# Optimization experiments

Measured on AMD Instinct MI355X. Metric: run time of the kernel, lower is better.

## Reference

```python
import jax, jax.numpy as jnp
import numpy as np

N_HEAD = 12
HEAD_DIM = 64
N_EMBD = 768
ATTN_MULT = 0.125
B, T = 2, 2048
NEG_INF = -1e30


def setup_inputs() -> dict:
    key = jax.random.key(0)
    ks = jax.random.split(key, 3)
    x = jax.random.normal(ks[0], (B, T, N_EMBD), dtype=jnp.float32)
    W_attn = jax.random.normal(ks[1], (N_EMBD, 3 * N_HEAD * HEAD_DIM), dtype=jnp.float32) * 0.02
    b_attn = jnp.zeros((3 * N_HEAD * HEAD_DIM,), dtype=jnp.float32)
    W_proj = jax.random.normal(ks[2], (N_HEAD * HEAD_DIM, N_EMBD), dtype=jnp.float32) * 0.02
    b_proj = jnp.zeros((N_EMBD,), dtype=jnp.float32)
    return {"x": x, "W_attn": W_attn, "b_attn": b_attn, "W_proj": W_proj, "b_proj": b_proj}


def reference(x, W_attn, b_attn, W_proj, b_proj):
    Bsz, Tlen, C = x.shape
    H, D = N_HEAD, HEAD_DIM
    qkv = x @ W_attn + b_attn                       # [B,T,3*H*D]
    q, k, v = jnp.split(qkv, 3, axis=-1)
    q = q.reshape(Bsz, Tlen, H, D).transpose(0, 2, 1, 3)   # [B,H,T,D]
    k = k.reshape(Bsz, Tlen, H, D).transpose(0, 2, 1, 3)
    v = v.reshape(Bsz, Tlen, H, D).transpose(0, 2, 1, 3)

    att = jnp.einsum('bhtd,bhsd->bhts', q, k) * ATTN_MULT  # [B,H,T,T]
    causal = jnp.tril(jnp.ones((Tlen, Tlen), dtype=bool))  # [T,T]
    att = jnp.where(causal, att, NEG_INF)

    # selection mask from head 0 (SelectionHeadLinearComboKind.NONE)
    S = jax.nn.relu(att[:, 0:1, :, :])                     # [B,1,T,T]; relu kills -inf
    # protect_bos_token: zero column 0 (key index 0)
    col = jnp.arange(Tlen)
    S = S * (col[None, None, None, :] != 0)
    # prevent_from_masking_myself: zero diagonal
    S = S * (1.0 - jnp.eye(Tlen, dtype=S.dtype))

    # accumulate selection over query (row) axis: ProtectionKind.NONE
    FF = jnp.cumsum(S, axis=-2)                            # [B,1,T,T]
    att = att - FF                                         # broadcast over heads

    p = jax.nn.softmax(att, axis=-1)                       # [B,H,T,T]
    y = jnp.einsum('bhts,bhsd->bhtd', p, v)                # [B,H,T,D]
    y = y.transpose(0, 2, 1, 3).reshape(Bsz, Tlen, H * D)  # [B,T,H*D]
    return y @ W_proj + b_proj
```

## Files before the change

kernel.cpp:

```cpp
#include <hip/hip_runtime.h>
#include <math.h>

#define T 2048
#define NH 12
#define HD 64
#define C3 2304
#define CE 768
#define NB 2

typedef __attribute__((ext_vector_type(8))) short bf16x8;
typedef __attribute__((ext_vector_type(4))) float f32x4;
typedef __attribute__((ext_vector_type(16))) float f32x16;
typedef __attribute__((ext_vector_type(4))) unsigned u32x4;

__device__ __forceinline__ void gload16(const void* g, void* l) {
    __builtin_amdgcn_global_load_lds(
        (const __attribute__((address_space(1))) void*)g,
        (__attribute__((address_space(3))) void*)l, 16, 0, 0);
}

__device__ inline void bf16split(float a, unsigned short& h, unsigned short& l) {
    unsigned int u = __float_as_uint(a);
    unsigned int r = (u + 0x7FFFu + ((u >> 16) & 1u)) >> 16;
    h = (unsigned short)r;
    float hf = __uint_as_float(r << 16);
    float lo = a - hf;
    unsigned int v = __float_as_uint(lo);
    l = (unsigned short)((v + 0x7FFFu + ((v >> 16) & 1u)) >> 16);
}

__device__ inline void packP(float a, float b, unsigned& wh, unsigned& wl) {
    unsigned short ha, la, hb, lb;
    bf16split(a, ha, la); bf16split(b, hb, lb);
    wh = (unsigned)ha | ((unsigned)hb << 16);
    wl = (unsigned)la | ((unsigned)lb << 16);
}

__global__ __launch_bounds__(256) void cvt_split_kernel(const float* __restrict__ A,
        unsigned short* __restrict__ H, unsigned short* __restrict__ L) {
    int i = blockIdx.x * 256 + threadIdx.x;
    float4 a0 = *(reinterpret_cast<const float4*>(A) + (size_t)i * 2);
    float4 a1 = *(reinterpret_cast<const float4*>(A) + (size_t)i * 2 + 1);
    float f[8] = {a0.x, a0.y, a0.z, a0.w, a1.x, a1.y, a1.z, a1.w};
    unsigned short h[8], l[8];
    #pragma unroll
    for (int j = 0; j < 8; ++j) bf16split(f[j], h[j], l[j]);
    uint4 hv, lv;
    hv.x = (unsigned)h[0] | ((unsigned)h[1] << 16); hv.y = (unsigned)h[2] | ((unsigned)h[3] << 16);
    hv.z = (unsigned)h[4] | ((unsigned)h[5] << 16); hv.w = (unsigned)h[6] | ((unsigned)h[7] << 16);
    lv.x = (unsigned)l[0] | ((unsigned)l[1] << 16); lv.y = (unsigned)l[2] | ((unsigned)l[3] << 16);
    lv.z = (unsigned)l[4] | ((unsigned)l[5] << 16); lv.w = (unsigned)l[6] | ((unsigned)l[7] << 16);
    reinterpret_cast<uint4*>(H)[i] = hv;
    reinterpret_cast<uint4*>(L)[i] = lv;
}

__global__ __launch_bounds__(256) void cvt_split_T_kernel(const float* __restrict__ W,
        unsigned short* __restrict__ H, unsigned short* __restrict__ L, int K, int N) {
    __shared__ float tile[64][65];
    const int n0 = blockIdx.x * 64, k0 = blockIdx.y * 64;
    const int t = threadIdx.x;
    {
        int r = t >> 2, c4 = (t & 3) * 16;
        #pragma unroll
        for (int u = 0; u < 4; ++u) {
            float4 w = *reinterpret_cast<const float4*>(&W[(size_t)(k0 + r) * N + n0 + c4 + u * 4]);
            tile[r][c4 + u * 4 + 0] = w.x; tile[r][c4 + u * 4 + 1] = w.y;
            tile[r][c4 + u * 4 + 2] = w.z; tile[r][c4 + u * 4 + 3] = w.w;
        }
    }
    __syncthreads();
    {
        int n = t >> 2, kc = (t & 3) * 16;
        unsigned short h[16], l[16];
        #pragma unroll
        for (int j = 0; j < 16; ++j) bf16split(tile[kc + j][n], h[j], l[j]);
        uint4 hv0, hv1, lv0, lv1;
        hv0.x = (unsigned)h[0] | ((unsigned)h[1] << 16);  hv0.y = (unsigned)h[2] | ((unsigned)h[3] << 16);
        hv0.z = (unsigned)h[4] | ((unsigned)h[5] << 16);  hv0.w = (unsigned)h[6] | ((unsigned)h[7] << 16);
        hv1.x = (unsigned)h[8] | ((unsigned)h[9] << 16);  hv1.y = (unsigned)h[10] | ((unsigned)h[11] << 16);
        hv1.z = (unsigned)h[12] | ((unsigned)h[13] << 16); hv1.w = (unsigned)h[14] | ((unsigned)h[15] << 16);
        lv0.x = (unsigned)l[0] | ((unsigned)l[1] << 16);  lv0.y = (unsigned)l[2] | ((unsigned)l[3] << 16);
        lv0.z = (unsigned)l[4] | ((unsigned)l[5] << 16);  lv0.w = (unsigned)l[6] | ((unsigned)l[7] << 16);
        lv1.x = (unsigned)l[8] | ((unsigned)l[9] << 16);  lv1.y = (unsigned)l[10] | ((unsigned)l[11] << 16);
        lv1.z = (unsigned)l[12] | ((unsigned)l[13] << 16); lv1.w = (unsigned)l[14] | ((unsigned)l[15] << 16);
        size_t o = (size_t)(n0 + n) * K + k0 + kc;
        reinterpret_cast<uint4*>(&H[o])[0] = hv0; reinterpret_cast<uint4*>(&H[o])[1] = hv1;
        reinterpret_cast<uint4*>(&L[o])[0] = lv0; reinterpret_cast<uint4*>(&L[o])[1] = lv1;
    }
}

__global__ __launch_bounds__(256) void cvt_kv_vt_kernel(const float* __restrict__ Vtmp,
        unsigned short* __restrict__ Vh, unsigned short* __restrict__ Vl) {
    __shared__ float tile[64][65];
    const int s0 = blockIdx.x * 64;
    const int bh = blockIdx.y;
    const int tid = threadIdx.x;
    {
        int r = tid >> 2, c0 = (tid & 3) * 16;
        const float* src = Vtmp + ((size_t)bh * T + s0 + r) * 64 + c0;
        #pragma unroll
        for (int u = 0; u < 4; ++u) {
            float4 w = *reinterpret_cast<const float4*>(src + u * 4);
            tile[r][c0 + u * 4 + 0] = w.x; tile[r][c0 + u * 4 + 1] = w.y;
            tile[r][c0 + u * 4 + 2] = w.z; tile[r][c0 + u * 4 + 3] = w.w;
        }
    }
    __syncthreads();
    {
        int d = tid >> 2, cs = (tid & 3) * 16;
        unsigned short hh[16], ll[16];
        #pragma unroll
        for (int j = 0; j < 16; ++j) bf16split(tile[cs + j][d], hh[j], ll[j]);
        uint4 hv0, hv1, lv0, lv1;
        hv0.x = (unsigned)hh[0] | ((unsigned)hh[1] << 16);  hv0.y = (unsigned)hh[2] | ((unsigned)hh[3] << 16);
        hv0.z = (unsigned)hh[4] | ((unsigned)hh[5] << 16);  hv0.w = (unsigned)hh[6] | ((unsigned)hh[7] << 16);
        hv1.x = (unsigned)hh[8] | ((unsigned)hh[9] << 16);  hv1.y = (unsigned)hh[10] | ((unsigned)hh[11] << 16);
        hv1.z = (unsigned)hh[12] | ((unsigned)hh[13] << 16); hv1.w = (unsigned)hh[14] | ((unsigned)hh[15] << 16);
        lv0.x = (unsigned)ll[0] | ((unsigned)ll[1] << 16);  lv0.y = (unsigned)ll[2] | ((unsigned)ll[3] << 16);
        lv0.z = (unsigned)ll[4] | ((unsigned)ll[5] << 16);  lv0.w = (unsigned)ll[6] | ((unsigned)ll[7] << 16);
        lv1.x = (unsigned)ll[8] | ((unsigned)ll[9] << 16);  lv1.y = (unsigned)ll[10] | ((unsigned)ll[11] << 16);
        lv1.z = (unsigned)ll[12] | ((unsigned)ll[13] << 16); lv1.w = (unsigned)ll[14] | ((unsigned)ll[15] << 16);
        size_t o = ((size_t)bh * 64 + d) * T + s0 + cs;
        reinterpret_cast<uint4*>(&Vh[o])[0] = hv0; reinterpret_cast<uint4*>(&Vh[o])[1] = hv1;
        reinterpret_cast<uint4*>(&Vl[o])[0] = lv0; reinterpret_cast<uint4*>(&Vl[o])[1] = lv1;
    }
}

#define LD32 32
__global__ __launch_bounds__(256) void gemm_mfma_kernel(
        const unsigned short* __restrict__ Ah, const unsigned short* __restrict__ Al,
        const unsigned short* __restrict__ Bh, const unsigned short* __restrict__ Bl,
        const float* __restrict__ bias, float* __restrict__ Cm,
        int M, int N, int K) {
    __shared__ unsigned short lA[2][128 * LD32];
    __shared__ unsigned short lB[2][128 * LD32];
    const int tid = threadIdx.x;
    const int nwg = gridDim.x * gridDim.y;
    int bid = blockIdx.y * gridDim.x + blockIdx.x;
    bid = (bid & 7) * (nwg >> 3) + (bid >> 3);
    const int bm = (bid / gridDim.x) * 128, bn = (bid % gridDim.x) * 128;
    const int lane = tid & 63, wid = tid >> 6;
    const int wr = wid >> 1, wc = wid & 1;
    f32x4 acc[4][4];
    #pragma unroll
    for (int i = 0; i < 4; ++i)
        #pragma unroll
        for (int j = 0; j < 4; ++j) acc[i][j] = (f32x4){0.f, 0.f, 0.f, 0.f};
    const int srow0 = wid * 32 + (lane >> 2);
    const int scn   = lane & 3;
    const int arb = wr * 64 + (lane & 15);
    const int brb = wc * 64 + (lane & 15);
    const int kc  = lane >> 4;
    for (int k0 = 0; k0 < K; k0 += 32) {
        __syncthreads();
        #pragma unroll
        for (int h = 0; h < 2; ++h) {
            int row = srow0 + h * 16;
            int cs = scn ^ ((row >> 1) & 3);
            size_t ao = (size_t)(bm + row) * K + k0 + cs * 8;
            size_t bo = (size_t)(bn + row) * K + k0 + cs * 8;
            unsigned short* d0 = &lA[0][(wid * 32 + h * 16) * LD32];
            unsigned short* d1 = &lA[1][(wid * 32 + h * 16) * LD32];
            unsigned short* d2 = &lB[0][(wid * 32 + h * 16) * LD32];
            unsigned short* d3 = &lB[1][(wid * 32 + h * 16) * LD32];
            gload16(&Ah[ao], d0);
            gload16(&Al[ao], d1);
            gload16(&Bh[bo], d2);
            gload16(&Bl[bo], d3);
        }
        __syncthreads();
        bf16x8 fa[2][4], fb[2][4];
        #pragma unroll
        for (int fi = 0; fi < 4; ++fi) {
            int ra = arb + fi * 16, rb = brb + fi * 16;
            int ca = (kc ^ ((ra >> 1) & 3)) * 8;
            int cb = (kc ^ ((rb >> 1) & 3)) * 8;
            fa[0][fi] = *reinterpret_cast<const bf16x8*>(&lA[0][ra * LD32 + ca]);
            fa[1][fi] = *reinterpret_cast<const bf16x8*>(&lA[1][ra * LD32 + ca]);
            fb[0][fi] = *reinterpret_cast<const bf16x8*>(&lB[0][rb * LD32 + cb]);
            fb[1][fi] = *reinterpret_cast<const bf16x8*>(&lB[1][rb * LD32 + cb]);
        }
        #pragma unroll
        for (int fi = 0; fi < 4; ++fi)
            #pragma unroll
            for (int fj = 0; fj < 4; ++fj) {
                acc[fi][fj] = __builtin_amdgcn_mfma_f32_16x16x32_bf16(fb[0][fj], fa[0][fi], acc[fi][fj], 0, 0, 0);
                acc[fi][fj] = __builtin_amdgcn_mfma_f32_16x16x32_bf16(fb[0][fj], fa[1][fi], acc[fi][fj], 0, 0, 0);
                acc[fi][fj] = __builtin_amdgcn_mfma_f32_16x16x32_bf16(fb[1][fj], fa[0][fi], acc[fi][fj], 0, 0, 0);
            }
    }
    const int mloc = lane & 15, ng = (lane >> 4) * 4;
    #pragma unroll
    for (int fi = 0; fi < 4; ++fi) {
        int row = bm + wr * 64 + fi * 16 + mloc;
        #pragma unroll
        for (int fj = 0; fj < 4; ++fj) {
            int n0 = bn + wc * 64 + fj * 16 + ng;
            float4 bv = *reinterpret_cast<const float4*>(&bias[n0]);
            float4 o4 = {acc[fi][fj][0] + bv.x, acc[fi][fj][1] + bv.y,
                         acc[fi][fj][2] + bv.z, acc[fi][fj][3] + bv.w};
            *reinterpret_cast<float4*>(&Cm[(size_t)row * N + n0]) = o4;
        }
    }
}

__global__ __launch_bounds__(256) void gemm_qkv_mfma_kernel(
        const unsigned short* __restrict__ Ah, const unsigned short* __restrict__ Al,
        const unsigned short* __restrict__ Bh, const unsigned short* __restrict__ Bl,
        const float* __restrict__ bias,
        unsigned short* __restrict__ Qh, unsigned short* __restrict__ Ql,
        unsigned short* __restrict__ Kh, unsigned short* __restrict__ Kl,
        float* __restrict__ Vtmp) {
    const int K = CE;
    __shared__ unsigned short lA[2][128 * LD32];
    __shared__ unsigned short lB[2][128 * LD32];
    const int tid = threadIdx.x;
    const int nwg = gridDim.x * gridDim.y;
    int bid = blockIdx.y * gridDim.x + blockIdx.x;
    bid = (bid & 7) * (nwg >> 3) + (bid >> 3);
    const int bm = (bid / gridDim.x) * 128, bn = (bid % gridDim.x) * 128;
    const int lane = tid & 63, wid = tid >> 6;
    const int wr = wid >> 1, wc = wid & 1;
    f32x4 acc[4][4];
    #pragma unroll
    for (int i = 0; i < 4; ++i)
        #pragma unroll
        for (int j = 0; j < 4; ++j) acc[i][j] = (f32x4){0.f, 0.f, 0.f, 0.f};
    const int srow0 = wid * 32 + (lane >> 2);
    const int scn   = lane & 3;
    const int arb = wr * 64 + (lane & 15);
    const int brb = wc * 64 + (lane & 15);
    const int kc  = lane >> 4;
    for (int k0 = 0; k0 < K; k0 += 32) {
        __syncthreads();
        #pragma unroll
        for (int h = 0; h < 2; ++h) {
            int row = srow0 + h * 16;
            int cs = scn ^ ((row >> 1) & 3);
            size_t ao = (size_t)(bm + row) * K + k0 + cs * 8;
            size_t bo = (size_t)(bn + row) * K + k0 + cs * 8;
            unsigned short* d0 = &lA[0][(wid * 32 + h * 16) * LD32];
            unsigned short* d1 = &lA[1][(wid * 32 + h * 16) * LD32];
            unsigned short* d2 = &lB[0][(wid * 32 + h * 16) * LD32];
            unsigned short* d3 = &lB[1][(wid * 32 + h * 16) * LD32];
            gload16(&Ah[ao], d0);
            gload16(&Al[ao], d1);
            gload16(&Bh[bo], d2);
            gload16(&Bl[bo], d3);
        }
        __syncthreads();
        bf16x8 fa[2][4], fb[2][4];
        #pragma unroll
        for (int fi = 0; fi < 4; ++fi) {
            int ra = arb + fi * 16, rb = brb + fi * 16;
            int ca = (kc ^ ((ra >> 1) & 3)) * 8;
            int cb = (kc ^ ((rb >> 1) & 3)) * 8;
            fa[0][fi] = *reinterpret_cast<const bf16x8*>(&lA[0][ra * LD32 + ca]);
            fa[1][fi] = *reinterpret_cast<const bf16x8*>(&lA[1][ra * LD32 + ca]);
            fb[0][fi] = *reinterpret_cast<const bf16x8*>(&lB[0][rb * LD32 + cb]);
            fb[1][fi] = *reinterpret_cast<const bf16x8*>(&lB[1][rb * LD32 + cb]);
        }
        #pragma unroll
        for (int fi = 0; fi < 4; ++fi)
            #pragma unroll
            for (int fj = 0; fj < 4; ++fj) {
                acc[fi][fj] = __builtin_amdgcn_mfma_f32_16x16x32_bf16(fb[0][fj], fa[0][fi], acc[fi][fj], 0, 0, 0);
                acc[fi][fj] = __builtin_amdgcn_mfma_f32_16x16x32_bf16(fb[0][fj], fa[1][fi], acc[fi][fj], 0, 0, 0);
                acc[fi][fj] = __builtin_amdgcn_mfma_f32_16x16x32_bf16(fb[1][fj], fa[0][fi], acc[fi][fj], 0, 0, 0);
            }
    }
    const int colbase = bn + wc * 64;
    const int region = colbase / 768;
    const int h = (colbase % 768) >> 6;
    const int mloc = lane & 15, ng = (lane >> 4) * 4;
    #pragma unroll
    for (int fi = 0; fi < 4; ++fi) {
        int tg = bm + wr * 64 + fi * 16 + mloc;
        int bb = tg >> 11, t = tg & (T - 1);
        #pragma unroll
        for (int fj = 0; fj < 4; ++fj) {
            int dbase = fj * 16 + ng;
            float4 bv = *reinterpret_cast<const float4*>(&bias[colbase + dbase]);
            float v0 = acc[fi][fj][0] + bv.x, v1 = acc[fi][fj][1] + bv.y;
            float v2 = acc[fi][fj][2] + bv.z, v3 = acc[fi][fj][3] + bv.w;
            size_t o = ((size_t)(bb * NH + h) * T + t) * 64 + dbase;
            if (region == 2) {
                float4 o4 = {v0, v1, v2, v3};
                *reinterpret_cast<float4*>(&Vtmp[o]) = o4;
            } else {
                unsigned short hh[4], ll[4];
                bf16split(v0, hh[0], ll[0]); bf16split(v1, hh[1], ll[1]);
                bf16split(v2, hh[2], ll[2]); bf16split(v3, hh[3], ll[3]);
                uint2 ph = {(unsigned)hh[0] | ((unsigned)hh[1] << 16),
                            (unsigned)hh[2] | ((unsigned)hh[3] << 16)};
                uint2 pl = {(unsigned)ll[0] | ((unsigned)ll[1] << 16),
                            (unsigned)ll[2] | ((unsigned)ll[3] << 16)};
                if (region == 0) {
                    *reinterpret_cast<uint2*>(&Qh[o]) = ph;
                    *reinterpret_cast<uint2*>(&Ql[o]) = pl;
                } else {
                    *reinterpret_cast<uint2*>(&Kh[o]) = ph;
                    *reinterpret_cast<uint2*>(&Kl[o]) = pl;
                }
            }
        }
    }
}

__global__ __launch_bounds__(256) void gemm_bias_kernel(
        const float* __restrict__ A, const float* __restrict__ B,
        const float* __restrict__ bias, float* __restrict__ Cm,
        int M, int N, int K) {
    __shared__ float As[16][64];
    __shared__ float Bs[16][68];
    const int tid = threadIdx.x;
    const int ty = tid >> 4, tx = tid & 15;
    const int bm = blockIdx.y * 64, bn = blockIdx.x * 64;
    float acc[4][4] = {};
    for (int k0 = 0; k0 < K; k0 += 16) {
        {
            int r = tid >> 2;
            int kk = (tid & 3) * 4;
            float4 a = *reinterpret_cast<const float4*>(&A[(size_t)(bm + r) * K + k0 + kk]);
            As[kk + 0][r] = a.x; As[kk + 1][r] = a.y; As[kk + 2][r] = a.z; As[kk + 3][r] = a.w;
        }
        {
            int kk = tid >> 4;
            int c = (tid & 15) * 4;
            *reinterpret_cast<float4*>(&Bs[kk][c]) =
                *reinterpret_cast<const float4*>(&B[(size_t)(k0 + kk) * N + bn + c]);
        }
        __syncthreads();
        #pragma unroll
        for (int kk = 0; kk < 16; ++kk) {
            float4 a4 = *reinterpret_cast<const float4*>(&As[kk][ty * 4]);
            float4 b4 = *reinterpret_cast<const float4*>(&Bs[kk][tx * 4]);
            float av[4] = {a4.x, a4.y, a4.z, a4.w};
            float bv[4] = {b4.x, b4.y, b4.z, b4.w};
            #pragma unroll
            for (int i = 0; i < 4; ++i)
                #pragma unroll
                for (int j = 0; j < 4; ++j)
                    acc[i][j] = fmaf(av[i], bv[j], acc[i][j]);
        }
        __syncthreads();
    }
    #pragma unroll
    for (int i = 0; i < 4; ++i) {
        int row = bm + ty * 4 + i;
        #pragma unroll
        for (int j = 0; j < 4; ++j) {
            int col = bn + tx * 4 + j;
            Cm[(size_t)row * N + col] = acc[i][j] + bias[col];
        }
    }
}

#define FST 72

__global__ __launch_bounds__(256) void s0_mfma_kernel(
        const unsigned short* __restrict__ Qh, const unsigned short* __restrict__ Ql,
        const unsigned short* __restrict__ Kh, const unsigned short* __restrict__ Kl,
        float* __restrict__ S, float* __restrict__ Psum) {
    const int kb = blockIdx.x * 64, qb = blockIdx.y * 64, b = blockIdx.z;
    const int tid = threadIdx.x;
    float* Sb = S + (size_t)b * T * T;
    if (kb > qb) {
        const int ty = tid >> 4, tx = tid & 15;
        #pragma unroll
        for (int i = 0; i < 4; ++i) {
            float4 z = {0.f, 0.f, 0.f, 0.f};
            *reinterpret_cast<float4*>(&Sb[(size_t)(qb + ty * 4 + i) * T + kb + tx * 4]) = z;
        }
        if (tid < 64) Psum[((size_t)(b * 32 + (qb >> 6)) * T) + kb + tid] = 0.f;
        return;
    }
    const int lane = tid & 63, w = tid >> 6;
    const int fr = lane & 15, fg = lane >> 4;
    __shared__ unsigned short Ks[2][64 * FST];
    __shared__ float csum[4][64];
    const int hb0 = b * NH;
    {
        const int sr = tid >> 2, sc0 = (tid & 3) * 16;
        const unsigned short* kh = Kh + ((size_t)hb0 * T + kb + sr) * 64 + sc0;
        const unsigned short* kl = Kl + ((size_t)hb0 * T + kb + sr) * 64 + sc0;
        uint4 a0 = reinterpret_cast<const uint4*>(kh)[0];
        uint4 a1 = reinterpret_cast<const uint4*>(kh)[1];
        uint4 b0 = reinterpret_cast<const uint4*>(kl)[0];
        uint4 b1 = reinterpret_cast<const uint4*>(kl)[1];
        *reinterpret_cast<uint4*>(&Ks[0][sr * FST + sc0 + 0]) = a0;
        *reinterpret_cast<uint4*>(&Ks[0][sr * FST + sc0 + 8]) = a1;
        *reinterpret_cast<uint4*>(&Ks[1][sr * FST + sc0 + 0]) = b0;
        *reinterpret_cast<uint4*>(&Ks[1][sr * FST + sc0 + 8]) = b1;
    }
    bf16x8 qh[2], ql[2];
    #pragma unroll
    for (int ks = 0; ks < 2; ++ks) {
        size_t qo = ((size_t)hb0 * T + qb + w * 16 + fr) * 64 + ks * 32 + fg * 8;
        qh[ks] = *reinterpret_cast<const bf16x8*>(&Qh[qo]);
        ql[ks] = *reinterpret_cast<const bf16x8*>(&Ql[qo]);
    }
    __syncthreads();
    f32x4 qk[4];
    #pragma unroll
    for (int fj = 0; fj < 4; ++fj) qk[fj] = (f32x4){0.f, 0.f, 0.f, 0.f};
    #pragma unroll
    for (int ks = 0; ks < 2; ++ks) {
        bf16x8 kbh[4], kbl[4];
        #pragma unroll
        for (int fj = 0; fj < 4; ++fj) {
            kbh[fj] = *reinterpret_cast<const bf16x8*>(&Ks[0][(fj * 16 + fr) * FST + ks * 32 + fg * 8]);
            kbl[fj] = *reinterpret_cast<const bf16x8*>(&Ks[1][(fj * 16 + fr) * FST + ks * 32 + fg * 8]);
        }
        #pragma unroll
        for (int fj = 0; fj < 4; ++fj) {
            qk[fj] = __builtin_amdgcn_mfma_f32_16x16x32_bf16(qh[ks], kbh[fj], qk[fj], 0, 0, 0);
            qk[fj] = __builtin_amdgcn_mfma_f32_16x16x32_bf16(qh[ks], kbl[fj], qk[fj], 0, 0, 0);
            qk[fj] = __builtin_amdgcn_mfma_f32_16x16x32_bf16(ql[ks], kbh[fj], qk[fj], 0, 0, 0);
        }
    }
    float colsum[4] = {0.f, 0.f, 0.f, 0.f};
    #pragma unroll
    for (int p = 0; p < 4; ++p) {
        int t = qb + w * 16 + fg * 4 + p;
        #pragma unroll
        for (int fj = 0; fj < 4; ++fj) {
            int s = kb + fj * 16 + fr;
            float v = qk[fj][p] * 0.125f;
            float o = (s >= 1 && s < t) ? fmaxf(v, 0.0f) : 0.0f;
            Sb[(size_t)t * T + s] = o;
            colsum[fj] += o;
        }
    }
    #pragma unroll
    for (int fj = 0; fj < 4; ++fj) {
        colsum[fj] += __shfl_xor(colsum[fj], 16);
        colsum[fj] += __shfl_xor(colsum[fj], 32);
    }
    if (lane < 16) {
        #pragma unroll
        for (int fj = 0; fj < 4; ++fj) csum[w][fj * 16 + lane] = colsum[fj];
    }
    __syncthreads();
    if (tid < 64) {
        float v = csum[0][tid] + csum[1][tid] + csum[2][tid] + csum[3][tid];
        Psum[((size_t)(b * 32 + (qb >> 6)) * T) + kb + tid] = v;
    }
}

__global__ __launch_bounds__(256) void s0_kernel(const float* __restrict__ qkv,
                                                 float* __restrict__ S) {
    const int kb = blockIdx.x * 64, qb = blockIdx.y * 64, b = blockIdx.z;
    const int tid = threadIdx.x, ty = tid >> 4, tx = tid & 15;
    float* Sb = S + (size_t)b * T * T;
    if (kb > qb) {
        #pragma unroll
        for (int i = 0; i < 4; ++i) {
            int row = qb + ty * 4 + i;
            float4 z = {0.f, 0.f, 0.f, 0.f};
            *reinterpret_cast<float4*>(&Sb[(size_t)row * T + kb + tx * 4]) = z;
        }
        return;
    }
    __shared__ float Qt[64][68];
    __shared__ float Kt[64][68];
    {
        int r = tid >> 2;
        int c0 = (tid & 3) * 16;
        const float* qrow = qkv + (size_t)(b * T + qb + r) * C3 + 0;
        const float* krow = qkv + (size_t)(b * T + kb + r) * C3 + 768;
        #pragma unroll
        for (int u = 0; u < 4; ++u) {
            float4 q4 = *reinterpret_cast<const float4*>(&qrow[c0 + u * 4]);
            float4 k4 = *reinterpret_cast<const float4*>(&krow[c0 + u * 4]);
            int d = c0 + u * 4;
            Qt[d + 0][r] = q4.x; Qt[d + 1][r] = q4.y; Qt[d + 2][r] = q4.z; Qt[d + 3][r] = q4.w;
            Kt[d + 0][r] = k4.x; Kt[d + 1][r] = k4.y; Kt[d + 2][r] = k4.z; Kt[d + 3][r] = k4.w;
        }
    }
    __syncthreads();
    float acc[4][4] = {};
    #pragma unroll
    for (int d = 0; d < 64; ++d) {
        float4 qv = *reinterpret_cast<const float4*>(&Qt[d][ty * 4]);
        float4 kv = *reinterpret_cast<const float4*>(&Kt[d][tx * 4]);
        float qa[4] = {qv.x, qv.y, qv.z, qv.w};
        float ka[4] = {kv.x, kv.y, kv.z, kv.w};
        #pragma unroll
        for (int i = 0; i < 4; ++i)
            #pragma unroll
            for (int j = 0; j < 4; ++j)
                acc[i][j] = fmaf(qa[i], ka[j], acc[i][j]);
    }
    #pragma unroll
    for (int i = 0; i < 4; ++i) {
        int t = qb + ty * 4 + i;
        float o[4];
        #pragma unroll
        for (int j = 0; j < 4; ++j) {
            int s = kb + tx * 4 + j;
            float v = acc[i][j] * 0.125f;
            o[j] = (s >= 1 && s < t) ? fmaxf(v, 0.0f) : 0.0f;
        }
        float4 o4 = {o[0], o[1], o[2], o[3]};
        *reinterpret_cast<float4*>(&Sb[(size_t)t * T + kb + tx * 4]) = o4;
    }
}

__global__ __launch_bounds__(256) void colsum_kernel(const float* __restrict__ S,
                                                     float* __restrict__ Psum) {
    int s = blockIdx.x * 256 + threadIdx.x;
    int j = blockIdx.y, b = blockIdx.z;
    const float* Sb = S + (size_t)b * T * T;
    float sum = 0.f;
    for (int r = 0; r < 64; ++r) sum += Sb[(size_t)(j * 64 + r) * T + s];
    Psum[((size_t)b * 32 + j) * T + s] = sum;
}

__global__ __launch_bounds__(256) void scanseg_kernel(float* __restrict__ Psum) {
    int s = blockIdx.x * 256 + threadIdx.x;
    int b = blockIdx.y;
    float v[32];
    #pragma unroll
    for (int j = 0; j < 32; ++j)
        v[j] = Psum[((size_t)(b * 32 + j)) * T + s];
    float run = 0.f;
    #pragma unroll
    for (int j = 0; j < 32; ++j) {
        Psum[((size_t)(b * 32 + j)) * T + s] = run;
        run += v[j];
    }
}

__global__ __launch_bounds__(256) void ffscan_kernel(float* __restrict__ S,
                                                     const float* __restrict__ Psum) {
    int s = blockIdx.x * 256 + threadIdx.x;
    int j = blockIdx.y, b = blockIdx.z;
    float run = Psum[((size_t)b * 32 + j) * T + s];
    float* Sb = S + (size_t)b * T * T;
    for (int r = 0; r < 64; ++r) {
        size_t idx = (size_t)(j * 64 + r) * T + s;
        run += Sb[idx];
        Sb[idx] = run;
    }
}

__device__ const int FTQ[40] = {15,15,15,15,14,14,14,13,13,13,12,12,12,11,11,11,10,10,9,9,8,8,7,7,6,5,4,3,14,10,6,2,13,9,5,1,12,8,4,0};
__device__ const int FK0[40] = {0,8,16,24,0,8,16,0,8,16,0,8,16,0,8,16,0,8,0,8,0,8,0,8,0,0,0,0,24,16,8,0,24,16,8,0,24,16,8,0};
__device__ const int FK1[40] = {8,16,24,32,8,16,24,8,16,24,8,16,24,8,16,24,8,16,8,16,8,16,8,16,8,8,8,8,30,22,14,6,28,20,12,4,26,18,10,2};
__device__ const int FCB[12] = {0,2,4,6,8,11,14,17,20,24,28,32};

__global__ __launch_bounds__(256) void flash_mfma_kernel(
        const unsigned short* __restrict__ Qh, const unsigned short* __restrict__ Ql,
        const unsigned short* __restrict__ Kh, const unsigned short* __restrict__ Kl,
        const unsigned short* __restrict__ Vth, const unsigned short* __restrict__ Vtl,
        const float* __restrict__ FF,
        unsigned short* __restrict__ Yh, unsigned short* __restrict__ Yl,
        float* __restrict__ PART) {
    const int hb = blockIdx.x;
    const int h = hb % NH, b = hb / NH;
    const int u = blockIdx.y;
    const int tq = FTQ[u], kt0 = FK0[u], kt1 = FK1[u];
    const int qb = tq * 128;
    const int tid = threadIdx.x;
    const int lane = tid & 63, w = tid >> 6;
    const int q31 = lane & 31, hi = lane >> 5;
    const int trow = qb + w * 32 + q31;
    __shared__ unsigned short KS[2][64 * FST];
    __shared__ unsigned short VS[2][64 * FST];

    bf16x8 qfh[4], qfl[4];
    #pragma unroll
    for (int dblk = 0; dblk < 4; ++dblk) {
        size_t qo = ((size_t)hb * T + trow) * 64 + dblk * 16 + hi * 8;
        qfh[dblk] = *reinterpret_cast<const bf16x8*>(&Qh[qo]);
        qfl[dblk] = *reinterpret_cast<const bf16x8*>(&Ql[qo]);
    }

    f32x16 oacc0 = (f32x16)(0.f), oacc1 = (f32x16)(0.f);
    float m = -1e30f, l = 0.f;
    const float* FFb = FF + (size_t)b * T * T;
    const int sr = tid >> 2, sc0 = (tid & 3) * 16;

    for (int kt = kt0; kt < kt1; ++kt) {
        const int kb = kt * 64;
        __syncthreads();
        {
            const unsigned short* ksrc = Kh + ((size_t)hb * T + kb + sr) * 64 + sc0;
            const unsigned short* ksrl = Kl + ((size_t)hb * T + kb + sr) * 64 + sc0;
            const unsigned short* vsrc = Vth + ((size_t)hb * 64 + sr) * T + kb + sc0;
            const unsigned short* vsrl = Vtl + ((size_t)hb * 64 + sr) * T + kb + sc0;
            uint4 k0v = reinterpret_cast<const uint4*>(ksrc)[0];
            uint4 k1v = reinterpret_cast<const uint4*>(ksrc)[1];
            uint4 k2v = reinterpret_cast<const uint4*>(ksrl)[0];
            uint4 k3v = reinterpret_cast<const uint4*>(ksrl)[1];
            uint4 v0v = reinterpret_cast<const uint4*>(vsrc)[0];
            uint4 v1v = reinterpret_cast<const uint4*>(vsrc)[1];
            uint4 v2v = reinterpret_cast<const uint4*>(vsrl)[0];
            uint4 v3v = reinterpret_cast<const uint4*>(vsrl)[1];
            *reinterpret_cast<uint4*>(&KS[0][sr * FST + sc0 + 0]) = k0v;
            *reinterpret_cast<uint4*>(&KS[0][sr * FST + sc0 + 8]) = k1v;
            *reinterpret_cast<uint4*>(&KS[1][sr * FST + sc0 + 0]) = k2v;
            *reinterpret_cast<uint4*>(&KS[1][sr * FST + sc0 + 8]) = k3v;
            *reinterpret_cast<uint4*>(&VS[0][sr * FST + sc0 + 0]) = v0v;
            *reinterpret_cast<uint4*>(&VS[0][sr * FST + sc0 + 8]) = v1v;
            *reinterpret_cast<uint4*>(&VS[1][sr * FST + sc0 + 0]) = v2v;
            *reinterpret_cast<uint4*>(&VS[1][sr * FST + sc0 + 8]) = v3v;
        }
        __syncthreads();
        f32x16 acc[2];
        acc[0] = (f32x16)(0.f); acc[1] = (f32x16)(0.f);
        #pragma unroll
        for (int sb = 0; sb < 2; ++sb) {
            #pragma unroll
            for (int dblk = 0; dblk < 4; ++dblk) {
                bf16x8 kfh = *reinterpret_cast<const bf16x8*>(&KS[0][(sb * 32 + q31) * FST + dblk * 16 + hi * 8]);
                bf16x8 kfl = *reinterpret_cast<const bf16x8*>(&KS[1][(sb * 32 + q31) * FST + dblk * 16 + hi * 8]);
                acc[sb] = __builtin_amdgcn_mfma_f32_32x32x16_bf16(kfh, qfh[dblk], acc[sb], 0, 0, 0);
                acc[sb] = __builtin_amdgcn_mfma_f32_32x32x16_bf16(kfh, qfl[dblk], acc[sb], 0, 0, 0);
                acc[sb] = __builtin_amdgcn_mfma_f32_32x32x16_bf16(kfl, qfh[dblk], acc[sb], 0, 0, 0);
            }
        }
        float pv[2][16];
        #pragma unroll
        for (int sb = 0; sb < 2; ++sb) {
            #pragma unroll
            for (int g = 0; g < 4; ++g) {
                float4 f4 = *reinterpret_cast<const float4*>(
                    &FFb[(size_t)trow * T + kb + sb * 32 + g * 8 + hi * 4]);
                float fv[4] = {f4.x, f4.y, f4.z, f4.w};
                #pragma unroll
                for (int a = 0; a < 4; ++a) {
                    int r = g * 4 + a;
                    int s = kb + sb * 32 + a + g * 8 + hi * 4;
                    float val = acc[sb][r] * 0.125f - fv[a];
                    pv[sb][r] = (s <= trow) ? val : -1e30f;
                }
            }
        }
        float tm = pv[0][0];
        #pragma unroll
        for (int sb = 0; sb < 2; ++sb)
            #pragma unroll
            for (int r = 0; r < 16; ++r) tm = fmaxf(tm, pv[sb][r]);
        tm = fmaxf(tm, __shfl_xor(tm, 32));
        float mn = fmaxf(m, tm);
        float scale = __expf(m - mn);
        float rs = 0.f;
        #pragma unroll
        for (int sb = 0; sb < 2; ++sb)
            #pragma unroll
            for (int r = 0; r < 16; ++r) {
                float pe = __expf(pv[sb][r] - mn);
                pv[sb][r] = pe; rs += pe;
            }
        rs += __shfl_xor(rs, 32);
        l = l * scale + rs;
        m = mn;
        oacc0 *= scale; oacc1 *= scale;
        unsigned wh[2][4][2], wl[2][4][2];
        #pragma unroll
        for (int sb = 0; sb < 2; ++sb)
            #pragma unroll
            for (int bq = 0; bq < 4; ++bq)
                #pragma unroll
                for (int h2 = 0; h2 < 2; ++h2)
                    packP(pv[sb][4 * bq + 2 * h2], pv[sb][4 * bq + 2 * h2 + 1],
                          wh[sb][bq][h2], wl[sb][bq][h2]);
        #pragma unroll
        for (int kk = 0; kk < 4; ++kk) {
            const int sb = kk >> 1;
            const int b0 = 2 * (kk & 1), b1 = b0 + 1;
            unsigned sh_b1_0 = (unsigned)__shfl_xor((int)wh[sb][b1][0], 32);
            unsigned sh_b1_1 = (unsigned)__shfl_xor((int)wh[sb][b1][1], 32);
            unsigned sh_b0_0 = (unsigned)__shfl_xor((int)wh[sb][b0][0], 32);
            unsigned sh_b0_1 = (unsigned)__shfl_xor((int)wh[sb][b0][1], 32);
            unsigned sl_b1_0 = (unsigned)__shfl_xor((int)wl[sb][b1][0], 32);
            unsigned sl_b1_1 = (unsigned)__shfl_xor((int)wl[sb][b1][1], 32);
            unsigned sl_b0_0 = (unsigned)__shfl_xor((int)wl[sb][b0][0], 32);
            unsigned sl_b0_1 = (unsigned)__shfl_xor((int)wl[sb][b0][1], 32);
            u32x4 th, tl;
            th[0] = hi ? sh_b1_0 : wh[sb][b0][0];
            th[1] = hi ? sh_b1_1 : wh[sb][b0][1];
            th[2] = hi ? wh[sb][b1][0] : sh_b0_0;
            th[3] = hi ? wh[sb][b1][1] : sh_b0_1;
            tl[0] = hi ? sl_b1_0 : wl[sb][b0][0];
            tl[1] = hi ? sl_b1_1 : wl[sb][b0][1];
            tl[2] = hi ? wl[sb][b1][0] : sl_b0_0;
            tl[3] = hi ? wl[sb][b1][1] : sl_b0_1;
            bf16x8 pbh = __builtin_bit_cast(bf16x8, th);
            bf16x8 pbl = __builtin_bit_cast(bf16x8, tl);
            {
                bf16x8 vfh = *reinterpret_cast<const bf16x8*>(&VS[0][(q31) * FST + kk * 16 + hi * 8]);
                bf16x8 vfl = *reinterpret_cast<const bf16x8*>(&VS[1][(q31) * FST + kk * 16 + hi * 8]);
                oacc0 = __builtin_amdgcn_mfma_f32_32x32x16_bf16(vfh, pbh, oacc0, 0, 0, 0);
                oacc0 = __builtin_amdgcn_mfma_f32_32x32x16_bf16(vfh, pbl, oacc0, 0, 0, 0);
                oacc0 = __builtin_amdgcn_mfma_f32_32x32x16_bf16(vfl, pbh, oacc0, 0, 0, 0);
            }
            {
                bf16x8 vfh = *reinterpret_cast<const bf16x8*>(&VS[0][(32 + q31) * FST + kk * 16 + hi * 8]);
                bf16x8 vfl = *reinterpret_cast<const bf16x8*>(&VS[1][(32 + q31) * FST + kk * 16 + hi * 8]);
                oacc1 = __builtin_amdgcn_mfma_f32_32x32x16_bf16(vfh, pbh, oacc1, 0, 0, 0);
                oacc1 = __builtin_amdgcn_mfma_f32_32x32x16_bf16(vfh, pbl, oacc1, 0, 0, 0);
                oacc1 = __builtin_amdgcn_mfma_f32_32x32x16_bf16(vfl, pbh, oacc1, 0, 0, 0);
            }
        }
    }
    if (tq < 4) {
        float inv = 1.f / l;
        size_t ybase = ((size_t)(b * T + trow)) * CE + h * 64;
        #pragma unroll
        for (int g = 0; g < 4; ++g) {
            unsigned short h0[4], l0[4], h1[4], l1[4];
            #pragma unroll
            for (int i = 0; i < 4; ++i) {
                bf16split(oacc0[4 * g + i] * inv, h0[i], l0[i]);
                bf16split(oacc1[4 * g + i] * inv, h1[i], l1[i]);
            }
            uint2 ph0 = {(unsigned)h0[0] | ((unsigned)h0[1] << 16), (unsigned)h0[2] | ((unsigned)h0[3] << 16)};
            uint2 pl0 = {(unsigned)l0[0] | ((unsigned)l0[1] << 16), (unsigned)l0[2] | ((unsigned)l0[3] << 16)};
            uint2 ph1 = {(unsigned)h1[0] | ((unsigned)h1[1] << 16), (unsigned)h1[2] | ((unsigned)h1[3] << 16)};
            uint2 pl1 = {(unsigned)l1[0] | ((unsigned)l1[1] << 16), (unsigned)l1[2] | ((unsigned)l1[3] << 16)};
            *reinterpret_cast<uint2*>(&Yh[ybase + g * 8 + hi * 4]) = ph0;
            *reinterpret_cast<uint2*>(&Yl[ybase + g * 8 + hi * 4]) = pl0;
            *reinterpret_cast<uint2*>(&Yh[ybase + 32 + g * 8 + hi * 4]) = ph1;
            *reinterpret_cast<uint2*>(&Yl[ybase + 32 + g * 8 + hi * 4]) = pl1;
        }
    } else {
        const int ci = FCB[tq - 4] + (kt0 >> 3);
        float* Ob = PART + (size_t)(hb * 36 + ci) * 8448;
        const int rr = w * 32 + q31;
        #pragma unroll
        for (int g = 0; g < 4; ++g) {
            float4 o0 = {oacc0[4 * g + 0], oacc0[4 * g + 1], oacc0[4 * g + 2], oacc0[4 * g + 3]};
            float4 o1 = {oacc1[4 * g + 0], oacc1[4 * g + 1], oacc1[4 * g + 2], oacc1[4 * g + 3]};
            *reinterpret_cast<float4*>(&Ob[rr * 64 + g * 8 + hi * 4]) = o0;
            *reinterpret_cast<float4*>(&Ob[rr * 64 + 32 + g * 8 + hi * 4]) = o1;
        }
        if (hi == 0) { Ob[8192 + rr] = m; Ob[8192 + 128 + rr] = l; }
    }
}

__global__ __launch_bounds__(256) void merge128_kernel(const float* __restrict__ PART,
                                                       unsigned short* __restrict__ Yh,
                                                       unsigned short* __restrict__ Yl) {
    const int hb = blockIdx.x;
    const int tq = 4 + blockIdx.y;
    const int h = hb % NH, b = hb / NH;
    const int nch = (tq >= 12) ? 4 : (tq >= 8) ? 3 : 2;
    const float* base = PART + (size_t)(hb * 36 + FCB[tq - 4]) * 8448;
    const int tid = threadIdx.x;
    const int r = tid >> 1, half = tid & 1;
    float mm[4], la[4];
    float M = -1e30f;
    #pragma unroll
    for (int c = 0; c < 4; ++c) {
        int cc = (c < nch) ? c : 0;
        float mv = base[(size_t)cc * 8448 + 8192 + r];
        float lv = base[(size_t)cc * 8448 + 8192 + 128 + r];
        mm[c] = (c < nch) ? mv : -1e30f;
        la[c] = (c < nch) ? lv : 0.f;
        M = fmaxf(M, mm[c]);
    }
    float a[4], L = 0.f;
    #pragma unroll
    for (int c = 0; c < 4; ++c) {
        a[c] = (c < nch) ? __expf(mm[c] - M) : 0.f;
        L += a[c] * la[c];
    }
    float inv = 1.f / L;
    const int t = tq * 128 + r;
    size_t ybase = ((size_t)(b * T + t)) * CE + h * 64 + half * 32;
    #pragma unroll
    for (int uu = 0; uu < 8; ++uu) {
        float ax = 0.f, ay = 0.f, az = 0.f, aw = 0.f;
        #pragma unroll
        for (int c = 0; c < 4; ++c) {
            int cc = (c < nch) ? c : 0;
            float4 x = *reinterpret_cast<const float4*>(
                &base[(size_t)cc * 8448 + r * 64 + half * 32 + uu * 4]);
            ax += a[c] * x.x; ay += a[c] * x.y; az += a[c] * x.z; aw += a[c] * x.w;
        }
        unsigned short hh[4], ll[4];
        bf16split(ax * inv, hh[0], ll[0]); bf16split(ay * inv, hh[1], ll[1]);
        bf16split(az * inv, hh[2], ll[2]); bf16split(aw * inv, hh[3], ll[3]);
        uint2 ph = {(unsigned)hh[0] | ((unsigned)hh[1] << 16), (unsigned)hh[2] | ((unsigned)hh[3] << 16)};
        uint2 pl = {(unsigned)ll[0] | ((unsigned)ll[1] << 16), (unsigned)ll[2] | ((unsigned)ll[3] << 16)};
        *reinterpret_cast<uint2*>(&Yh[ybase + uu * 4]) = ph;
        *reinterpret_cast<uint2*>(&Yl[ybase + uu * 4]) = pl;
    }
}

__global__ __launch_bounds__(256) void flash_kernel(const float* __restrict__ qkv,
                                                    const float* __restrict__ FF,
                                                    float* __restrict__ Y,
                                                    float* __restrict__ PO,
                                                    float* __restrict__ PML,
                                                    int split) {
    const int hb = blockIdx.x;
    const int h = hb % NH, b = hb / NH;
    int qt, kt0, kt1, mode;
    if (split) {
        const int u = blockIdx.y;
        if (u < 16)      { qt = 16 + u; kt0 = 0;  kt1 = 16;     mode = 1; }
        else if (u < 32) { qt = 31 - u; kt0 = 0;  kt1 = qt + 1; mode = 0; }
        else             { qt = 63 - u; kt0 = 16; kt1 = qt + 1; mode = 2; }
    } else {
        qt = 31 - blockIdx.y; kt0 = 0; kt1 = qt + 1; mode = 0;
    }
    const int qb = qt * 64;
    const int tid = threadIdx.x, ty = tid >> 4, tx = tid & 15;
    __shared__ float Qt[64][68];
    __shared__ float KtPs[64][68];
    __shared__ float Vs[64][68];
    const int r = tid >> 2, c0 = (tid & 3) * 16;
    {
        const float* qrow = qkv + (size_t)(b * T + qb + r) * C3 + h * 64;
        #pragma unroll
        for (int u = 0; u < 4; ++u) {
            float4 q4 = *reinterpret_cast<const float4*>(&qrow[c0 + u * 4]);
            int d = c0 + u * 4;
            Qt[d + 0][r] = q4.x; Qt[d + 1][r] = q4.y; Qt[d + 2][r] = q4.z; Qt[d + 3][r] = q4.w;
        }
    }
    float m[4], l[4], O[4][4];
    #pragma unroll
    for (int i = 0; i < 4; ++i) {
        m[i] = -1e30f; l[i] = 0.f;
        #pragma unroll
        for (int j = 0; j < 4; ++j) O[i][j] = 0.f;
    }
    const float* FFb = FF + (size_t)b * T * T;
    for (int kt = kt0; kt < kt1; ++kt) {
        const int kb = kt * 64;
        __syncthreads();
        {
            const float* krow = qkv + (size_t)(b * T + kb + r) * C3 + 768 + h * 64;
            const float* vrow = qkv + (size_t)(b * T + kb + r) * C3 + 1536 + h * 64;
            #pragma unroll
            for (int u = 0; u < 4; ++u) {
                float4 k4 = *reinterpret_cast<const float4*>(&krow[c0 + u * 4]);
                int d = c0 + u * 4;
                KtPs[d + 0][r] = k4.x; KtPs[d + 1][r] = k4.y;
                KtPs[d + 2][r] = k4.z; KtPs[d + 3][r] = k4.w;
                *reinterpret_cast<float4*>(&Vs[r][c0 + u * 4]) =
                    *reinterpret_cast<const float4*>(&vrow[c0 + u * 4]);
            }
        }
        __syncthreads();
        float sc[4][4] = {};
        #pragma unroll
        for (int d = 0; d < 64; ++d) {
            float4 qv = *reinterpret_cast<const float4*>(&Qt[d][ty * 4]);
            float4 kv = *reinterpret_cast<const float4*>(&KtPs[d][tx * 4]);
            float qa[4] = {qv.x, qv.y, qv.z, qv.w};
            float ka[4] = {kv.x, kv.y, kv.z, kv.w};
            #pragma unroll
            for (int i = 0; i < 4; ++i)
                #pragma unroll
                for (int j = 0; j < 4; ++j)
                    sc[i][j] = fmaf(qa[i], ka[j], sc[i][j]);
        }
        #pragma unroll
        for (int i = 0; i < 4; ++i) {
            int t = qb + ty * 4 + i;
            float4 f4 = *reinterpret_cast<const float4*>(&FFb[(size_t)t * T + kb + tx * 4]);
            float fv[4] = {f4.x, f4.y, f4.z, f4.w};
            #pragma unroll
            for (int j = 0; j < 4; ++j) {
                int s = kb + tx * 4 + j;
                float v = sc[i][j] * 0.125f - fv[j];
                sc[i][j] = (s <= t) ? v : -1e30f;
            }
        }
        #pragma unroll
        for (int i = 0; i < 4; ++i) {
            float tm = fmaxf(fmaxf(sc[i][0], sc[i][1]), fmaxf(sc[i][2], sc[i][3]));
            tm = fmaxf(tm, __shfl_xor(tm, 1));
            tm = fmaxf(tm, __shfl_xor(tm, 2));
            tm = fmaxf(tm, __shfl_xor(tm, 4));
            tm = fmaxf(tm, __shfl_xor(tm, 8));
            float mn = fmaxf(m[i], tm);
            float scale = __expf(m[i] - mn);
            float rs = 0.f;
            #pragma unroll
            for (int j = 0; j < 4; ++j) {
                float p = __expf(sc[i][j] - mn);
                sc[i][j] = p; rs += p;
            }
            rs += __shfl_xor(rs, 1); rs += __shfl_xor(rs, 2);
            rs += __shfl_xor(rs, 4); rs += __shfl_xor(rs, 8);
            l[i] = l[i] * scale + rs;
            m[i] = mn;
            #pragma unroll
            for (int j = 0; j < 4; ++j) O[i][j] *= scale;
        }
        __syncthreads();
        #pragma unroll
        for (int i = 0; i < 4; ++i) {
            float4 p4 = {sc[i][0], sc[i][1], sc[i][2], sc[i][3]};
            *reinterpret_cast<float4*>(&KtPs[ty * 4 + i][tx * 4]) = p4;
        }
        __syncthreads();
        #pragma unroll
        for (int j4 = 0; j4 < 16; ++j4) {
            float pvv[4][4];
            #pragma unroll
            for (int i = 0; i < 4; ++i) {
                float4 t4 = *reinterpret_cast<const float4*>(&KtPs[ty * 4 + i][j4 * 4]);
                pvv[i][0] = t4.x; pvv[i][1] = t4.y; pvv[i][2] = t4.z; pvv[i][3] = t4.w;
            }
            #pragma unroll
            for (int jj = 0; jj < 4; ++jj) {
                float4 v4 = *reinterpret_cast<const float4*>(&Vs[j4 * 4 + jj][tx * 4]);
                float vv[4] = {v4.x, v4.y, v4.z, v4.w};
                #pragma unroll
                for (int i = 0; i < 4; ++i)
                    #pragma unroll
                    for (int dd = 0; dd < 4; ++dd)
                        O[i][dd] = fmaf(pvv[i][jj], vv[dd], O[i][dd]);
            }
        }
    }
    if (mode == 0) {
        #pragma unroll
        for (int i = 0; i < 4; ++i) {
            int t = qb + ty * 4 + i;
            float inv = 1.f / l[i];
            float4 o4 = {O[i][0] * inv, O[i][1] * inv, O[i][2] * inv, O[i][3] * inv};
            *reinterpret_cast<float4*>(&Y[(size_t)(b * T + t) * CE + h * 64 + tx * 4]) = o4;
        }
    } else {
        const int pidx = (b * NH + h) * 16 + (qt - 16);
        float* Ob  = PO  + (size_t)(mode - 1) * (NB * NH * 16 * 4096) + (size_t)pidx * 4096;
        float* mlb = PML + (size_t)(mode - 1) * (NB * NH * 16 * 128)  + (size_t)pidx * 128;
        #pragma unroll
        for (int i = 0; i < 4; ++i) {
            int rr = ty * 4 + i;
            float4 o4 = {O[i][0], O[i][1], O[i][2], O[i][3]};
            *reinterpret_cast<float4*>(&Ob[rr * 64 + tx * 4]) = o4;
            if (tx == 0) { mlb[rr] = m[i]; mlb[64 + rr] = l[i]; }
        }
    }
}

__global__ __launch_bounds__(256) void merge_kernel(const float* __restrict__ PO,
                                                    const float* __restrict__ PML,
                                                    float* __restrict__ Y) {
    const int p = blockIdx.x;
    const int q16 = p & 15;
    const int hb = p >> 4;
    const int h = hb % NH, b = hb / NH;
    const int qt = 16 + q16;
    const float* O0  = PO  + (size_t)p * 4096;
    const float* O1  = PO  + (size_t)(NB * NH * 16) * 4096 + (size_t)p * 4096;
    const float* ml0 = PML + (size_t)p * 128;
    const float* ml1 = PML + (size_t)(NB * NH * 16) * 128  + (size_t)p * 128;
    const int tid = threadIdx.x;
    const int r = tid >> 2, c0 = (tid & 3) * 16;
    float m0 = ml0[r], l0 = ml0[64 + r];
    float m1 = ml1[r], l1 = ml1[64 + r];
    float M  = fmaxf(m0, m1);
    float a0 = __expf(m0 - M), a1 = __expf(m1 - M);
    float inv = 1.f / (a0 * l0 + a1 * l1);
    const int t = qt * 64 + r;
    float* Yrow = Y + (size_t)(b * T + t) * CE + h * 64;
    #pragma unroll
    for (int u = 0; u < 4; ++u) {
        float4 x0 = *reinterpret_cast<const float4*>(&O0[r * 64 + c0 + u * 4]);
        float4 x1 = *reinterpret_cast<const float4*>(&O1[r * 64 + c0 + u * 4]);
        float4 y;
        y.x = (a0 * x0.x + a1 * x1.x) * inv;
        y.y = (a0 * x0.y + a1 * x1.y) * inv;
        y.z = (a0 * x0.z + a1 * x1.z) * inv;
        y.w = (a0 * x0.w + a1 * x1.w) * inv;
        *reinterpret_cast<float4*>(&Yrow[c0 + u * 4]) = y;
    }
}

extern "C" void kernel_launch(void* const* d_in, const int* in_sizes, int n_in,
                              void* d_out, int out_size, void* d_ws, size_t ws_size,
                              hipStream_t stream) {
    const float* x      = (const float*)d_in[0];
    const float* W_attn = (const float*)d_in[1];
    const float* b_attn = (const float*)d_in[2];
    const float* W_proj = (const float*)d_in[3];
    const float* b_proj = (const float*)d_in[4];
    float* out = (float*)d_out;

    char* ws = (char*)d_ws;
    const size_t QKV_BYTES = (size_t)NB * T * C3 * 4;
    const size_t S_BYTES   = (size_t)NB * T * T * 4;
    const size_t P_BYTES   = (size_t)NB * 32 * T * 4;
    const size_t Y_BYTES   = (size_t)NB * T * CE * 4;
    const size_t PO_BYTES  = (size_t)2 * NB * NH * 16 * 4096 * 4;
    const size_t PML_BYTES = (size_t)2 * NB * NH * 16 * 128 * 4;
    const size_t PLANE_X   = (size_t)NB * T * CE * 2;
    const size_t PLANE_WA  = (size_t)C3 * CE * 2;
    const size_t PLANE_WP  = (size_t)CE * CE * 2;
    const size_t PLANE_KV  = (size_t)NB * NH * T * 64 * 2;

    const size_t U_OFF  = QKV_BYTES + S_BYTES + P_BYTES + Y_BYTES;
    const size_t U_SIZE = PO_BYTES + PML_BYTES;
    const size_t W_OFF  = U_OFF + U_SIZE;
    const size_t KV_OFF = W_OFF + 2 * PLANE_WA + 2 * PLANE_WP;

    float* qkv  = (float*)ws;
// ... 75 lines not shown
```

Before: 246.4 us.

## Overlap FF loads with QK MFMAs, truncate P split, batch ffscan loads

Splits the QK^T MFMA loop into two halves and issues the FF tile global loads between them, so load latency hides under matrix work. It brackets MFMA groups with s_setprio to favour matrix issue. It replaces the round-to-nearest bf16 hi/lo split of P with a truncation-based split that needs fewer integer ops. It also batches eight loads before the stores in the ffscan column scan to expose memory parallelism. Truncating the hi part changes rounding slightly, but the lo term still carries the residual.

```diff
diff --git a/kernel.cpp b/kernel.cpp
--- a/kernel.cpp
+++ b/kernel.cpp
@@ -29,11 +29,13 @@
     l = (unsigned short)((v + 0x7FFFu + ((v >> 16) & 1u)) >> 16);
 }
 
-__device__ inline void packP(float a, float b, unsigned& wh, unsigned& wl) {
-    unsigned short ha, la, hb, lb;
-    bf16split(a, ha, la); bf16split(b, hb, lb);
-    wh = (unsigned)ha | ((unsigned)hb << 16);
-    wl = (unsigned)la | ((unsigned)lb << 16);
+__device__ inline void packPfast(float a, float b, unsigned& wh, unsigned& wl) {
+    unsigned ua = __float_as_uint(a), ub = __float_as_uint(b);
+    unsigned ha = ua >> 16, hb = ub & 0xFFFF0000u;
+    float la = a - __uint_as_float(ha << 16);
+    float lb = b - __uint_as_float(hb);
+    wh = ha | hb;
+    wl = (__float_as_uint(la) >> 16) | (__float_as_uint(lb) & 0xFFFF0000u);
 }
 
 __global__ __launch_bounds__(256) void cvt_split_kernel(const float* __restrict__ A,
@@ -538,10 +540,16 @@
     int j = blockIdx.y, b = blockIdx.z;
     float run = Psum[((size_t)b * 32 + j) * T + s];
     float* Sb = S + (size_t)b * T * T;
-    for (int r = 0; r < 64; ++r) {
-        size_t idx = (size_t)(j * 64 + r) * T + s;
-        run += Sb[idx];
-        Sb[idx] = run;
+    for (int r0 = 0; r0 < 64; r0 += 8) {
+        float v[8];
+        #pragma unroll
+        for (int i = 0; i < 8; ++i)
+            v[i] = Sb[(size_t)(j * 64 + r0 + i) * T + s];
+        #pragma unroll
+        for (int i = 0; i < 8; ++i) {
+            run += v[i];
+            Sb[(size_t)(j * 64 + r0 + i) * T + s] = run;
+        }
     }
 }
 
@@ -608,34 +616,48 @@
             *reinterpret_cast<uint4*>(&VS[1][sr * FST + sc0 + 8]) = v3v;
         }
         __syncthreads();
-        f32x16 acc[2];
-        acc[0] = (f32x16)(0.f); acc[1] = (f32x16)(0.f);
-        #pragma unroll
-        for (int sb = 0; sb < 2; ++sb) {
-            #pragma unroll
-            for (int dblk = 0; dblk < 4; ++dblk) {
-                bf16x8 kfh = *reinterpret_cast<const bf16x8*>(&KS[0][(sb * 32 + q31) * FST + dblk * 16 + hi * 8]);
-                bf16x8 kfl = *reinterpret_cast<const bf16x8*>(&KS[1][(sb * 32 + q31) * FST + dblk * 16 + hi * 8]);
-                acc[sb] = __builtin_amdgcn_mfma_f32_32x32x16_bf16(kfh, qfh[dblk], acc[sb], 0, 0, 0);
-                acc[sb] = __builtin_amdgcn_mfma_f32_32x32x16_bf16(kfh, qfl[dblk], acc[sb], 0, 0, 0);
-                acc[sb] = __builtin_amdgcn_mfma_f32_32x32x16_bf16(kfl, qfh[dblk], acc[sb], 0, 0, 0);
-            }
-        }
+        f32x16 acc0 = (f32x16)(0.f), acc1 = (f32x16)(0.f);
+        __builtin_amdgcn_s_setprio(1);
+        #pragma unroll
+        for (int dblk = 0; dblk < 4; ++dblk) {
+            bf16x8 kfh = *reinterpret_cast<const bf16x8*>(&KS[0][(q31) * FST + dblk * 16 + hi * 8]);
+            bf16x8 kfl = *reinterpret_cast<const bf16x8*>(&KS[1][(q31) * FST + dblk * 16 + hi * 8]);
+            acc0 = __builtin_amdgcn_mfma_f32_32x32x16_bf16(kfh, qfh[dblk], acc0, 0, 0, 0);
+            acc0 = __builtin_amdgcn_mfma_f32_32x32x16_bf16(kfh, qfl[dblk], acc0, 0, 0, 0);
+            acc0 = __builtin_amdgcn_mfma_f32_32x32x16_bf16(kfl, qfh[dblk], acc0, 0, 0, 0);
+        }
+        __builtin_amdgcn_s_setprio(0);
+        float4 ffv[2][4];
+        #pragma unroll
+        for (int sb = 0; sb < 2; ++sb)
+            #pragma unroll
+            for (int g = 0; g < 4; ++g)
+                ffv[sb][g] = *reinterpret_cast<const float4*>(
+                    &FFb[(size_t)trow * T + kb + sb * 32 + g * 8 + hi * 4]);
+        __builtin_amdgcn_s_setprio(1);
+        #pragma unroll
+        for (int dblk = 0; dblk < 4; ++dblk) {
+            bf16x8 kfh = *reinterpret_cast<const bf16x8*>(&KS[0][(32 + q31) * FST + dblk * 16 + hi * 8]);
+            bf16x8 kfl = *reinterpret_cast<const bf16x8*>(&KS[1][(32 + q31) * FST + dblk * 16 + hi * 8]);
+            acc1 = __builtin_amdgcn_mfma_f32_32x32x16_bf16(kfh, qfh[dblk], acc1, 0, 0, 0);
+            acc1 = __builtin_amdgcn_mfma_f32_32x32x16_bf16(kfh, qfl[dblk], acc1, 0, 0, 0);
+            acc1 = __builtin_amdgcn_mfma_f32_32x32x16_bf16(kfl, qfh[dblk], acc1, 0, 0, 0);
+        }
+        __builtin_amdgcn_s_setprio(0);
         float pv[2][16];
         #pragma unroll
-        for (int sb = 0; sb < 2; ++sb) {
-            #pragma unroll
-            for (int g = 0; g < 4; ++g) {
-                float4 f4 = *reinterpret_cast<const float4*>(
-                    &FFb[(size_t)trow * T + kb + sb * 32 + g * 8 + hi * 4]);
-                float fv[4] = {f4.x, f4.y, f4.z, f4.w};
-                #pragma unroll
-                for (int a = 0; a < 4; ++a) {
-                    int r = g * 4 + a;
-                    int s = kb + sb * 32 + a + g * 8 + hi * 4;
-                    float val = acc[sb][r] * 0.125f - fv[a];
-                    pv[sb][r] = (s <= trow) ? val : -1e30f;
-                }
+        for (int g = 0; g < 4; ++g) {
+            float fv0[4] = {ffv[0][g].x, ffv[0][g].y, ffv[0][g].z, ffv[0][g].w};
+            float fv1[4] = {ffv[1][g].x, ffv[1][g].y, ffv[1][g].z, ffv[1][g].w};
+            #pragma unroll
+            for (int a = 0; a < 4; ++a) {
+                int r = g * 4 + a;
+                int s0i = kb + a + g * 8 + hi * 4;
+                int s1i = s0i + 32;
+                float v0 = acc0[r] * 0.125f - fv0[a];
+                float v1 = acc1[r] * 0.125f - fv1[a];
+                pv[0][r] = (s0i <= trow) ? v0 : -1e30f;
+                pv[1][r] = (s1i <= trow) ? v1 : -1e30f;
             }
         }
         float tm = pv[0][0];
@@ -665,8 +687,8 @@
             for (int bq = 0; bq < 4; ++bq)
                 #pragma unroll
                 for (int h2 = 0; h2 < 2; ++h2)
-                    packP(pv[sb][4 * bq + 2 * h2], pv[sb][4 * bq + 2 * h2 + 1],
-                          wh[sb][bq][h2], wl[sb][bq][h2]);
+                    packPfast(pv[sb][4 * bq + 2 * h2], pv[sb][4 * bq + 2 * h2 + 1],
+                              wh[sb][bq][h2], wl[sb][bq][h2]);
         #pragma unroll
         for (int kk = 0; kk < 4; ++kk) {
             const int sb = kk >> 1;
@@ -693,16 +715,20 @@
             {
                 bf16x8 vfh = *reinterpret_cast<const bf16x8*>(&VS[0][(q31) * FST + kk * 16 + hi * 8]);
                 bf16x8 vfl = *reinterpret_cast<const bf16x8*>(&VS[1][(q31) * FST + kk * 16 + hi * 8]);
+                __builtin_amdgcn_s_setprio(1);
                 oacc0 = __builtin_amdgcn_mfma_f32_32x32x16_bf16(vfh, pbh, oacc0, 0, 0, 0);
                 oacc0 = __builtin_amdgcn_mfma_f32_32x32x16_bf16(vfh, pbl, oacc0, 0, 0, 0);
                 oacc0 = __builtin_amdgcn_mfma_f32_32x32x16_bf16(vfl, pbh, oacc0, 0, 0, 0);
+                __builtin_amdgcn_s_setprio(0);
             }
             {
                 bf16x8 vfh = *reinterpret_cast<const bf16x8*>(&VS[0][(32 + q31) * FST + kk * 16 + hi * 8]);
                 bf16x8 vfl = *reinterpret_cast<const bf16x8*>(&VS[1][(32 + q31) * FST + kk * 16 + hi * 8]);
+                __builtin_amdgcn_s_setprio(1);
                 oacc1 = __builtin_amdgcn_mfma_f32_32x32x16_bf16(vfh, pbh, oacc1, 0, 0, 0);
                 oacc1 = __builtin_amdgcn_mfma_f32_32x32x16_bf16(vfh, pbl, oacc1, 0, 0, 0);
                 oacc1 = __builtin_amdgcn_mfma_f32_32x32x16_bf16(vfl, pbh, oacc1, 0, 0, 0);
+                __builtin_amdgcn_s_setprio(0);
             }
         }
     }
```

After: 247.4 us. No clear change (+0.4%).
